# Optimization experiments

Measured on AMD Instinct MI355X. Metric: run time of the kernel, lower is better.

Reference implementation:

```python
import jax, jax.numpy as jnp
import numpy as np

EPS = 2e-5
N_ROT = 4  # p4 group: rotations by multiples of 90 degrees (exact via rot90)


def _conv2d(x, w, pad):
    # x: [B, Cin, H, W], w: [Cout, Cin, k, k]
    return jax.lax.conv_general_dilated(
        x, w, window_strides=(1, 1), padding=[(pad, pad), (pad, pad)],
        dimension_numbers=('NCHW', 'OIHW', 'NCHW'))


def _conv_rng(x, w):
    # Lifting (Rn -> G) conv. x: [B, I, H, W], w: [O, I, k, k] -> [B, O, 4, H', W']
    O, I, k, _ = w.shape
    wr = jnp.stack([jnp.rot90(w, r, axes=(-2, -1)) for r in range(N_ROT)])  # [4,O,I,k,k]
    y = _conv2d(x, wr.reshape(N_ROT * O, I, k, k), 0)  # [B, 4*O, H', W']
    B, _, H2, W2 = y.shape
    return y.reshape(B, N_ROT, O, H2, W2).transpose(0, 2, 1, 3, 4)


def _conv_gg(x, w, pad=0):
    # Group (G -> G) conv. x: [B, I, 4, H, W], w: [O, I, 4, k, k] -> [B, O, 4, H', W']
    O, I, _, k, _ = w.shape
    ws = []
    for r in range(N_ROT):
        wr = jnp.rot90(w, r, axes=(-2, -1))      # spatial rotation of the kernel
        wr = jnp.roll(wr, r, axis=2)              # cyclic shift of orientation axis
        ws.append(wr.reshape(O, I * N_ROT, k, k))
    wall = jnp.concatenate(ws, 0)                 # [4*O, I*4, k, k]
    B = x.shape[0]
    y = _conv2d(x.reshape(B, I * N_ROT, x.shape[-2], x.shape[-1]), wall, pad)
    H2, W2 = y.shape[-2:]
    return y.reshape(B, N_ROT, O, H2, W2).transpose(0, 2, 1, 3, 4)


def _att_rng(x, aw):
    # fSpatialAttention on Rn input: channel avg+max pooling -> 7x7 conv -> sigmoid gate.
    # x: [B, C, H, W], aw: [1, 2, 7, 7]
    pooled = jnp.concatenate([x.mean(1, keepdims=True), x.max(1, keepdims=True)], axis=1)
    att = jax.nn.sigmoid(_conv2d(pooled, aw, 3))  # [B,1,H,W], SAME padding
    return x * att


def _att_gg(x, aw):
    # fSpatialAttentionGG on G input: channel avg+max pooling -> equivariant 7x7 GG conv -> sigmoid.
    # x: [B, C, 4, H, W], aw: [1, 2, 4, 7, 7]
    pooled = jnp.concatenate([x.mean(1, keepdims=True), x.max(1, keepdims=True)], axis=1)
    att = jax.nn.sigmoid(_conv_gg(pooled, aw, pad=3))  # [B,1,4,H,W]
    return x * att


def _bn(x, g, b):
    # BatchNorm3d over [B, C, 4, H, W]: per-channel stats over (B, 4, H, W)
    m = x.mean((0, 2, 3, 4), keepdims=True)
    v = x.var((0, 2, 3, 4), keepdims=True)
    return (x - m) * jax.lax.rsqrt(v + EPS) * g.reshape(1, -1, 1, 1, 1) + b.reshape(1, -1, 1, 1, 1)


def _pool(x):
    # max_pooling_Rn: 2x2/2 spatial max pool applied independently per orientation
    return jax.lax.reduce_window(x, -jnp.inf, jax.lax.max,
                                 (1, 1, 1, 2, 2), (1, 1, 1, 2, 2), 'VALID')


def setup_inputs() -> dict:
    key = jax.random.key(0)
    ks = jax.random.split(key, 40)
    B, C = 2048, 10
    d = {'x': jax.random.normal(ks[0], (B, 1, 28, 28), jnp.float32)}
    d['c1_w'] = 0.2 * jax.random.normal(ks[1], (C, 1, 3, 3), jnp.float32)
    d['a1_w'] = 0.1 * jax.random.normal(ks[2], (1, 2, 7, 7), jnp.float32)
    j = 3
    for i in range(2, 7):
        d['c%d_w' % i] = 0.1 * jax.random.normal(ks[j], (C, C, 4, 3, 3), jnp.float32); j += 1
        d['a%d_w' % i] = 0.1 * jax.random.normal(ks[j], (1, 2, 4, 7, 7), jnp.float32); j += 1
    d['c7_w'] = 0.1 * jax.random.normal(ks[j], (10, C, 4, 4, 4), jnp.float32); j += 1
    d['a7_w'] = 0.1 * jax.random.normal(ks[j], (1, 2, 4, 7, 7), jnp.float32); j += 1
    for i in range(1, 7):
        d['bn%d_g' % i] = jnp.ones((C,), jnp.float32)
        d['bn%d_b' % i] = jnp.zeros((C,), jnp.float32)
    return d


def reference(x, c1_w, a1_w, c2_w, a2_w, c3_w, a3_w, c4_w, a4_w, c5_w, a5_w,
              c6_w, a6_w, c7_w, a7_w, bn1_g, bn1_b, bn2_g, bn2_b, bn3_g, bn3_b,
              bn4_g, bn4_b, bn5_g, bn5_b, bn6_g, bn6_b):
    # Dropout is treated as identity (eval mode / deterministic reference).
    out = jax.nn.relu(_bn(_conv_rng(_att_rng(x, a1_w), c1_w), bn1_g, bn1_b))      # [B,10,4,26,26]
    out = jax.nn.relu(_bn(_conv_gg(_att_gg(out, a2_w), c2_w), bn2_g, bn2_b))       # [B,10,4,24,24]
    out = _pool(out)                                                                # [B,10,4,12,12]
    out = jax.nn.relu(_bn(_conv_gg(_att_gg(out, a3_w), c3_w), bn3_g, bn3_b))       # 10x10
    out = jax.nn.relu(_bn(_conv_gg(_att_gg(out, a4_w), c4_w), bn4_g, bn4_b))       # 8x8
    out = jax.nn.relu(_bn(_conv_gg(_att_gg(out, a5_w), c5_w), bn5_g, bn5_b))       # 6x6
    out = jax.nn.relu(_bn(_conv_gg(_att_gg(out, a6_w), c6_w), bn6_g, bn6_b))       # 4x4
    out = _conv_gg(_att_gg(out, a7_w), c7_w)                                        # [B,10,4,1,1]
    out = out.max(axis=2)                                                           # group max-pool over orientations
    return out.reshape(out.shape[0], 10)
```

## Files before the change

kernel.cpp:

```cpp
#include <hip/hip_runtime.h>
#include <hip/hip_bf16.h>
#include <cstddef>

typedef __hip_bfloat16 bf;
typedef __attribute__((ext_vector_type(8))) short short8x;
typedef __attribute__((ext_vector_type(4))) float f32x4;

__device__ __forceinline__ float ldv(const float* p){ return *p; }
__device__ __forceinline__ float ldv(const bf* p){ return __bfloat162float(*p); }
__device__ __forceinline__ void stv(float* p, float v){ *p = v; }
__device__ __forceinline__ void stv(bf* p, float v){ *p = __float2bfloat16(v); }
__device__ __forceinline__ float sigm(float x){ return 1.f/(1.f + __expf(-x)); }
__device__ __forceinline__ short bfbits(float v){
  __hip_bfloat16 h = __float2bfloat16(v);
  return *(short*)&h;
}

__device__ __forceinline__ float ldin(const void* p, long i, int f32){
  return f32 ? ((const float*)p)[i] : __bfloat162float(((const bf*)p)[i]);
}

template<int K>
__device__ __forceinline__ int rot_src(int r, int t){
  int u = t / K, v = t % K;
  int s1 = v*K + (K-1-u);
  int s2 = (K-1-u)*K + (K-1-v);
  int s3 = (K-1-v)*K + u;
  return r==0 ? t : (r==1 ? s1 : (r==2 ? s2 : s3));
}

__global__ void k_detect(const void* x, int* ctrl){
  int lane = threadIdx.x;
  float mx = 0.f;
  for (int i = lane; i < 2048; i += 64){
    float v = __bfloat162float(((const bf*)x)[i]);
    if (v != v) v = 1e30f;
    mx = fmaxf(mx, fabsf(v));
  }
  #pragma unroll
  for (int off = 32; off > 0; off >>= 1) mx = fmaxf(mx, __shfl_xor(mx, off));
  if (lane == 0) ctrl[0] = (mx > 1e6f) ? 1 : 0;
}

__global__ __launch_bounds__(256) void k_build_bt(const void* c2, const void* c3, const void* c4,
                                                  const int* __restrict__ ctrl, short* __restrict__ btg){
  const void* ws[3] = {c2, c3, c4};
  const void* cw = ws[blockIdx.x];
  short* outp = btg + blockIdx.x * 17280;
  int f32 = ctrl[0];
  for (int i = threadIdx.x; i < 17280; i += 256){
    int t, n, k;
    if (i < 13824){
      t = i / 1536;
      int rem = i % 1536;
      int kq = rem / 384;
      n = (rem >> 3) % 48;
      k = kq*8 + (i & 7);
    } else {
      int j = i - 13824;
      t = j / 384;
      n = (j >> 3) % 48;
      k = 32 + (j & 7);
    }
    float v = 0.f;
    if (n < 40 && k < 40){
      int o = n >> 2, r = n & 3, ci = k >> 2, s = k & 3;
      v = ldin(cw, ((o*10 + ci)*4 + ((s - r) & 3))*9 + rot_src<3>(r, t), f32);
    }
    outp[i] = bfbits(v);
  }
}

__global__ __launch_bounds__(256) void k_l1(const void* __restrict__ x,
                                            const void* __restrict__ a1,
                                            const void* __restrict__ c1,
                                            const int* __restrict__ ctrl,
                                            float* __restrict__ xa,
                                            float* __restrict__ ssum, float* __restrict__ ssq){
  __shared__ float xs[784];
  __shared__ float ws[49];
  __shared__ float xg[28*29];
  __shared__ float wr1[360];
  __shared__ float lsum[16], lss[16];
  int b = blockIdx.x, tid = threadIdx.x;
  int f32 = ctrl[0];
  for (int i = tid; i < 784; i += 256) xs[i] = ldin(x, (long)b*784 + i, f32);
  if (tid < 49) ws[tid] = ldin(a1, tid, f32) + ldin(a1, 49 + tid, f32);
  for (int i = tid; i < 360; i += 256){
    int r = i / 90, rem = i % 90, o = rem / 9, t = rem % 9;
    wr1[i] = ldin(c1, o*9 + rot_src<3>(r, t), f32);
  }
  if (tid < 16){ lsum[tid] = 0.f; lss[tid] = 0.f; }
  __syncthreads();
  for (int p = tid; p < 784; p += 256){
    int h = p / 28, w = p % 28;
    float acc = 0.f;
    #pragma unroll
    for (int u = 0; u < 7; ++u){
      int hh = h + u - 3;
      if (hh < 0 || hh >= 28) continue;
      #pragma unroll
      for (int v = 0; v < 7; ++v){
        int ww = w + v - 3;
        if (ww < 0 || ww >= 28) continue;
        acc = fmaf(xs[hh*28 + ww], ws[u*7 + v], acc);
      }
    }
    float g = xs[p] * sigm(acc);
    xg[h*29 + w] = g;
    xa[(size_t)b*784 + p] = g;
  }
  __syncthreads();
  for (int it = tid; it < 1040; it += 256){
    int o = it / 104, rem = it % 104, r = rem / 26, h = rem % 26;
    float wt[9];
    #pragma unroll
    for (int t = 0; t < 9; ++t) wt[t] = wr1[(r*10 + o)*9 + t];
    float acc[26];
    #pragma unroll
    for (int w = 0; w < 26; ++w) acc[w] = 0.f;
    #pragma unroll
    for (int u = 0; u < 3; ++u){
      float rr[28];
      #pragma unroll
      for (int j = 0; j < 28; ++j) rr[j] = xg[(h + u)*29 + j];
      #pragma unroll
      for (int v = 0; v < 3; ++v){
        float wv = wt[u*3 + v];
        #pragma unroll
        for (int w = 0; w < 26; ++w) acc[w] = fmaf(rr[w + v], wv, acc[w]);
      }
    }
    float s1 = 0.f, s2 = 0.f;
    #pragma unroll
    for (int w = 0; w < 26; ++w){ s1 += acc[w]; s2 += acc[w]*acc[w]; }
    atomicAdd(&lsum[o], s1); atomicAdd(&lss[o], s2);
  }
  __syncthreads();
  if (tid < 10){ atomicAdd(&ssum[tid], lsum[tid]); atomicAdd(&ssq[tid], lss[tid]); }
}

__global__ void k_finalize(const float* __restrict__ ssum, const float* __restrict__ ssq,
                           const void* __restrict__ g, const void* __restrict__ bb,
                           const int* __restrict__ ctrl,
                           float invN, float* __restrict__ scale, float* __restrict__ shift){
  int c = threadIdx.x;
  if (c < 10){
    float m = ssum[c] * invN;
    float v = fmaxf(ssq[c] * invN - m*m, 0.f);
    float sc = ldin(g, c, ctrl[0]) * rsqrtf(v + 2e-5f);
    scale[c] = sc;
    shift[c] = ldin(bb, c, ctrl[0]) - m * sc;
  }
}

__global__ __launch_bounds__(128) void k_att2(const float* __restrict__ xa,
                                              const void* __restrict__ c1,
                                              const float* __restrict__ sc1,
                                              const float* __restrict__ sh1,
                                              const void* __restrict__ aw,
                                              const int* __restrict__ ctrl,
                                              float* __restrict__ attf){
  __shared__ float xs[28*29];
  __shared__ float wr1[360];
  __shared__ float ps[8*26*33];
  __shared__ float wl[1568];
  __shared__ float scs[10], shs[10];
  int b = blockIdx.x, tid = threadIdx.x;
  int f32 = ctrl[0];
  for (int i = tid; i < 784; i += 128){
    int row = i / 28, col = i % 28;
    xs[row*29 + col] = xa[(size_t)b*784 + i];
  }
  for (int i = tid; i < 360; i += 128){
    int r = i / 90, rem = i % 90, o = rem / 9, t = rem % 9;
    wr1[i] = ldin(c1, o*9 + rot_src<3>(r, t), f32);
  }
  for (int i = tid; i < 8*26*33; i += 128) ps[i] = 0.f;
  for (int i = tid; i < 1568; i += 128){
    int r = i / 392, rem = i % 392, i2 = rem / 196, s = (rem % 196)/49, t = rem % 49;
    int sp = (s - r) & 3;
    wl[i] = ldin(aw, (i2*4 + sp)*49 + rot_src<7>(r, t), f32);
  }
  if (tid < 10){ scs[tid] = sc1[tid]; shs[tid] = sh1[tid]; }
  __syncthreads();
  if (tid < 104){
    int s = tid / 26, h = tid % 26;
    float msum[26], mmax[26];
    #pragma unroll
    for (int w = 0; w < 26; ++w){ msum[w] = 0.f; mmax[w] = 0.f; }
    for (int o = 0; o < 10; ++o){
      const float* wb = wr1 + (s*10 + o)*9;
      float acc[26];
      #pragma unroll
      for (int w = 0; w < 26; ++w) acc[w] = 0.f;
      #pragma unroll
      for (int u = 0; u < 3; ++u){
        float rr[28];
        #pragma unroll
        for (int j = 0; j < 28; ++j) rr[j] = xs[(h + u)*29 + j];
        #pragma unroll
        for (int v = 0; v < 3; ++v){
          float wv = wb[u*3 + v];
          #pragma unroll
          for (int w = 0; w < 26; ++w) acc[w] = fmaf(rr[w + v], wv, acc[w]);
        }
      }
      float a_sc = scs[o], a_sh = shs[o];
      #pragma unroll
      for (int w = 0; w < 26; ++w){
        float val = fmaxf(fmaf(acc[w], a_sc, a_sh), 0.f);
        msum[w] += val; mmax[w] = fmaxf(mmax[w], val);
      }
    }
    #pragma unroll
    for (int w = 0; w < 26; ++w){
      ps[s*858 + h*33 + 3 + w] = msum[w] * 0.1f;
      ps[(4 + s)*858 + h*33 + 3 + w] = mmax[w];
    }
  }
  __syncthreads();
  if (tid < 104){
    int r = tid / 26, h = tid % 26;
    float acc[26];
    #pragma unroll
    for (int w = 0; w < 26; ++w) acc[w] = 0.f;
    for (int c = 0; c < 8; ++c){
      const float* wb = wl + r*392 + c*49;
      const float* pb = ps + c*858;
      #pragma unroll
      for (int u = 0; u < 7; ++u){
        int row = h + u - 3;
        if (row < 0 || row >= 26) continue;
        float rr[32];
        #pragma unroll
        for (int j = 0; j < 32; ++j) rr[j] = pb[row*33 + j];
        #pragma unroll
        for (int v = 0; v < 7; ++v){
          float wv = wb[u*7 + v];
          #pragma unroll
          for (int w = 0; w < 26; ++w) acc[w] = fmaf(rr[w + v], wv, acc[w]);
        }
      }
    }
    size_t base = ((size_t)b*4 + r)*676 + (size_t)h*26;
    #pragma unroll
    for (int w = 0; w < 26; ++w) attf[base + w] = sigm(acc[w]);
  }
}

__global__ __launch_bounds__(512, 4) void k_conv2m(const float* __restrict__ xa,
                                                const void* __restrict__ c1,
                                                const float* __restrict__ sc1,
                                                const float* __restrict__ sh1,
                                                const float* __restrict__ attm,
                                                const short* __restrict__ btg,
                                                const int* __restrict__ ctrl,
                                                bf* __restrict__ ap2,
                                                float* __restrict__ ssum, float* __restrict__ ssq){
  __shared__ alignas(16) float xs2[784];
  __shared__ float wr1[360];
  __shared__ alignas(16) float attL[4*676];
  __shared__ alignas(16) short xin[676*40];
  __shared__ float lsum[16], lss[16];
  int tid = threadIdx.x, b = blockIdx.x;
  int f32 = ctrl[0];
  for (int i = tid; i < 784; i += 512) xs2[i] = xa[(size_t)b*784 + i];
  for (int i = tid; i < 360; i += 512){
    int r = i / 90, rem = i % 90, o = rem / 9, t = rem % 9;
    wr1[i] = ldin(c1, o*9 + rot_src<3>(r, t), f32);
  }
  for (int i = tid; i < 2704; i += 512) attL[i] = attm[(size_t)b*2704 + i];
  if (tid < 16){ lsum[tid] = 0.f; lss[tid] = 0.f; }
  __syncthreads();
  for (int it = tid; it < 1040; it += 512){
    int row = it / 40, ch = it % 40;
    int ci = ch >> 2, s = ch & 3;
    float wt[9];
    {
      const float* wb = wr1 + (s*10 + ci)*9;
      #pragma unroll
      for (int t = 0; t < 9; ++t) wt[t] = wb[t];
    }
    float sc = sc1[ci], sh = sh1[ci];
    float acc[26];
    #pragma unroll
    for (int w = 0; w < 26; ++w) acc[w] = 0.f;
    #pragma unroll
    for (int u = 0; u < 3; ++u){
      float rr[28];
      const float4* rp = (const float4*)(xs2 + (row + u)*28);
      #pragma unroll
      for (int j = 0; j < 7; ++j){ float4 q = rp[j]; rr[4*j]=q.x; rr[4*j+1]=q.y; rr[4*j+2]=q.z; rr[4*j+3]=q.w; }
      #pragma unroll
      for (int v = 0; v < 3; ++v){
        float wv = wt[u*3 + v];
        #pragma unroll
        for (int w = 0; w < 26; ++w) acc[w] = fmaf(rr[w + v], wv, acc[w]);
      }
    }
    const float* ap = attL + s*676 + row*26;
    #pragma unroll
    for (int w = 0; w < 26; ++w){
      float v = fmaxf(fmaf(acc[w], sc, sh), 0.f) * ap[w];
      xin[(row*26 + w)*40 + ch] = bfbits(v);
    }
  }
  __syncthreads();

  int wv = tid >> 6, lane = tid & 63, lm = lane & 15, lq = lane >> 4;
  short8x z8 = {0,0,0,0,0,0,0,0};
  short8x b32[9], bt1[9];
  int curNt = -1, n = 0, o = 0;
  for (int u = wv; u < 54; u += 8){
    int nt = u / 18, mp = u % 18;
    if (nt != curNt){
      curNt = nt; n = nt*16 + lm; o = n >> 2;
      #pragma unroll
      for (int t = 0; t < 9; ++t){
        b32[t] = *(const short8x*)(btg + (((t*4 + lq)*48 + n) << 3));
        bt1[t] = z8;
        if (lq == 0) bt1[t] = *(const short8x*)(btg + 13824 + ((t*48 + n) << 3));
      }
    }
    int mt0 = mp*2, mt1 = mp*2 + 1;
    int mA0 = mt0*16 + lm, mA1 = mt1*16 + lm;
    int qi0 = mA0 >> 2, sub0 = mA0 & 3;
    int h00 = 2*(qi0/12) + (sub0 >> 1), w00 = 2*(qi0%12) + (sub0 & 1);
    int qi1 = mA1 >> 2, sub1 = mA1 & 3;
    int h01 = 2*(qi1/12) + (sub1 >> 1), w01 = 2*(qi1%12) + (sub1 & 1);
    f32x4 acc0 = {0.f,0.f,0.f,0.f}, acc1 = {0.f,0.f,0.f,0.f};
    #pragma unroll
    for (int t = 0; t < 9; ++t){
      int sp0 = (h00 + t/3)*26 + (w00 + t%3);
      int sp1 = (h01 + t/3)*26 + (w01 + t%3);
      short8x a00 = *(const short8x*)&xin[sp0*40 + lq*8];
      short8x a01 = *(const short8x*)&xin[sp1*40 + lq*8];
      short8x a10 = z8, a11 = z8;
      if (lq == 0){
        a10 = *(const short8x*)&xin[sp0*40 + 32];
        a11 = *(const short8x*)&xin[sp1*40 + 32];
      }
      acc0 = __builtin_amdgcn_mfma_f32_16x16x32_bf16(a00, b32[t], acc0, 0, 0, 0);
      acc1 = __builtin_amdgcn_mfma_f32_16x16x32_bf16(a01, b32[t], acc1, 0, 0, 0);
      acc0 = __builtin_amdgcn_mfma_f32_16x16x32_bf16(a10, bt1[t], acc0, 0, 0, 0);
      acc1 = __builtin_amdgcn_mfma_f32_16x16x32_bf16(a11, bt1[t], acc1, 0, 0, 0);
    }
    if (n < 40){
      float s1 = acc0[0]+acc0[1]+acc0[2]+acc0[3] + acc1[0]+acc1[1]+acc1[2]+acc1[3];
      float s2 = acc0[0]*acc0[0]+acc0[1]*acc0[1]+acc0[2]*acc0[2]+acc0[3]*acc0[3]
               + acc1[0]*acc1[0]+acc1[1]*acc1[1]+acc1[2]*acc1[2]+acc1[3]*acc1[3];
      atomicAdd(&lsum[o], s1); atomicAdd(&lss[o], s2);
      float mx0 = fmaxf(fmaxf(acc0[0], acc0[1]), fmaxf(acc0[2], acc0[3]));
      float mx1 = fmaxf(fmaxf(acc1[0], acc1[1]), fmaxf(acc1[2], acc1[3]));
      size_t pbase = ((size_t)b*40 + n)*144;
      stv(ap2 + pbase + mt0*4 + lq, mx0);
      stv(ap2 + pbase + mt1*4 + lq, mx1);
    }
  }
  __syncthreads();
  if (tid < 10){ atomicAdd(&ssum[tid], lsum[tid]); atomicAdd(&ssq[tid], lss[tid]); }
}

template<int HIN, int WIN, int NT, typename TI>
__global__ __launch_bounds__(NT) void k_conv_ggm(const TI* __restrict__ act,
                                                 const float* __restrict__ scale,
                                                 const float* __restrict__ shift,
                                                 const float* __restrict__ attm,
                                                 const short* __restrict__ btg,
                                                 float* __restrict__ out,
                                                 float* __restrict__ ssum, float* __restrict__ ssq){
  constexpr int HOUT = HIN - 2, WOUT = WIN - 2;
  constexpr int M = HOUT*WOUT, HW = HIN*WIN;
  constexpr int MT = (M + 15)/16, MU = (MT + 1)/2, UNITS = MU*3;
  constexpr int NWV = NT/64;
  __shared__ alignas(16) short xin[HW*40];
  __shared__ float lsum[16], lss[16];
  int tid = threadIdx.x, b = blockIdx.x;
  if (tid < 16){ lsum[tid] = 0.f; lss[tid] = 0.f; }
  for (int i = tid; i < HW*40; i += NT){
    int sp = i / 40, ch = i % 40;
    int ci = ch >> 2, s = ch & 3;
    float a = ldv(act + ((size_t)b*40 + ch)*HW + sp);
    a = fmaxf(fmaf(a, scale[ci], shift[ci]), 0.f);
    xin[i] = bfbits(a * attm[((size_t)b*4 + s)*HW + sp]);
  }
  __syncthreads();
  int wv = tid >> 6, lane = tid & 63, lm = lane & 15, lq = lane >> 4;
  short8x z8 = {0,0,0,0,0,0,0,0};
  short8x b32[9], bt1[9];
  int curNt = -1, n = 0, o = 0;
  for (int u = wv; u < UNITS; u += NWV){
    int nt = u / MU, mu = u % MU;
    if (nt != curNt){
      curNt = nt; n = nt*16 + lm; o = n >> 2;
      #pragma unroll
      for (int t = 0; t < 9; ++t){
        b32[t] = *(const short8x*)(btg + (((t*4 + lq)*48 + n) << 3));
        bt1[t] = z8;
        if (lq == 0) bt1[t] = *(const short8x*)(btg + 13824 + ((t*48 + n) << 3));
      }
    }
    int mt0 = mu*2, mt1 = mu*2 + 1;
    int mA0 = mt0*16 + lm; if (mA0 > M-1) mA0 = M-1;
    int mA1 = mt1*16 + lm; if (mA1 > M-1) mA1 = M-1;
    int mh0 = mA0 / WOUT, mw0 = mA0 % WOUT;
    int mh1 = mA1 / WOUT, mw1 = mA1 % WOUT;
    f32x4 acc0 = {0.f,0.f,0.f,0.f}, acc1 = {0.f,0.f,0.f,0.f};
    #pragma unroll
    for (int t = 0; t < 9; ++t){
      int sp0 = (mh0 + t/3)*WIN + (mw0 + t%3);
      int sp1 = (mh1 + t/3)*WIN + (mw1 + t%3);
      short8x a00 = *(const short8x*)&xin[sp0*40 + lq*8];
      short8x a01 = *(const short8x*)&xin[sp1*40 + lq*8];
      short8x a10 = z8, a11 = z8;
      if (lq == 0){
        a10 = *(const short8x*)&xin[sp0*40 + 32];
        a11 = *(const short8x*)&xin[sp1*40 + 32];
      }
      acc0 = __builtin_amdgcn_mfma_f32_16x16x32_bf16(a00, b32[t], acc0, 0, 0, 0);
      acc1 = __builtin_amdgcn_mfma_f32_16x16x32_bf16(a01, b32[t], acc1, 0, 0, 0);
      acc0 = __builtin_amdgcn_mfma_f32_16x16x32_bf16(a10, bt1[t], acc0, 0, 0, 0);
      acc1 = __builtin_amdgcn_mfma_f32_16x16x32_bf16(a11, bt1[t], acc1, 0, 0, 0);
    }
    if (n < 40){
      float s1 = 0.f, s2 = 0.f;
      size_t obase = ((size_t)b*40 + n)*M;
      #pragma unroll
      for (int reg = 0; reg < 4; ++reg){
        int m0 = mt0*16 + lq*4 + reg;
        if (m0 < M){ float v = acc0[reg]; s1 += v; s2 += v*v; out[obase + m0] = v; }
        int m1 = mt1*16 + lq*4 + reg;
        if (m1 < M){ float v = acc1[reg]; s1 += v; s2 += v*v; out[obase + m1] = v; }
      }
      atomicAdd(&lsum[o], s1); atomicAdd(&lss[o], s2);
    }
  }
  __syncthreads();
  if (tid < 10){ atomicAdd(&ssum[tid], lsum[tid]); atomicAdd(&ssq[tid], lss[tid]); }
}

template<int H, int W, int NT, typename TA>
__global__ __launch_bounds__(NT) void k_att_gg(const TA* __restrict__ act,
                                               const float* __restrict__ scale,
                                               const float* __restrict__ shift,
                                               const void* __restrict__ aw,
                                               const int* __restrict__ ctrl,
                                               float* __restrict__ att){
  constexpr int WG = (W + 6) | 1;
  constexpr int HW = H*W;
  __shared__ float ps[8*H*WG];
  __shared__ float wl[1568];
  int b = blockIdx.x, tid = threadIdx.x;
  int f32 = ctrl[0];
  for (int i = tid; i < 4*H*WG; i += NT){
    int s = i / (H*WG), rem = i % (H*WG), row = rem / WG, col = rem % WG;
    int cc = col - 3;
    float mn = 0.f, mx = 0.f;
    if (cc >= 0 && cc < W){
      float sum = 0.f; mx = 0.f;
      const TA* ap = act + (size_t)b*40*HW + (size_t)s*HW + row*W + cc;
      #pragma unroll
      for (int c = 0; c < 10; ++c){
        float v = fmaxf(fmaf(ldv(ap + (size_t)c*4*HW), scale[c], shift[c]), 0.f);
        sum += v; mx = fmaxf(mx, v);
      }
      mn = sum * 0.1f;
    }
    ps[s*H*WG + row*WG + col] = mn;
    ps[(4 + s)*H*WG + row*WG + col] = mx;
  }
  for (int i = tid; i < 1568; i += NT){
    int r = i / 392, rem = i % 392, i2 = rem / 196, s = (rem % 196)/49, t = rem % 49;
    int sp = (s - r) & 3;
    wl[i] = ldin(aw, (i2*4 + sp)*49 + rot_src<7>(r, t), f32);
  }
  __syncthreads();
  for (int it = tid; it < 4*H; it += NT){
    int r = it / H, h = it % H;
    float acc[W];
    #pragma unroll
    for (int w = 0; w < W; ++w) acc[w] = 0.f;
    for (int c = 0; c < 8; ++c){
      const float* wb = wl + r*392 + c*49;
      const float* pb = ps + c*H*WG;
      #pragma unroll
      for (int u = 0; u < 7; ++u){
        int row = h + u - 3;
        if (row < 0 || row >= H) continue;
        float rr[W + 6];
        #pragma unroll
        for (int j = 0; j < W + 6; ++j) rr[j] = pb[row*WG + j];
        #pragma unroll
        for (int v = 0; v < 7; ++v){
          float wv = wb[u*7 + v];
          #pragma unroll
          for (int w = 0; w < W; ++w) acc[w] = fmaf(rr[w + v], wv, acc[w]);
        }
      }
    }
    size_t base = ((size_t)b*4 + r)*HW + (size_t)h*W;
    #pragma unroll
    for (int w = 0; w < W; ++w) att[base + w] = sigm(acc[w]);
  }
}

template<int HIN, int WIN, int K, int SR, int NT, bool STATS, typename TI, typename TO>
__global__ __launch_bounds__(NT) void k_conv_gg(const TI* __restrict__ act,
                                                const float* __restrict__ scale,
                                                const float* __restrict__ shift,
                                                const float* __restrict__ attm,
                                                const void* __restrict__ cw,
                                                const int* __restrict__ ctrl,
                                                TO* __restrict__ out,
                                                float* __restrict__ ssum, float* __restrict__ ssq){
  constexpr int HOUT = HIN - K + 1;
  constexpr int WOUT = WIN - K + 1;
  constexpr int NS   = HOUT / SR;
  constexpr int WP   = WIN | 1;
  constexpr int NW   = 10*10*4*K*K;
  __shared__ float xin[40*HIN*WP];
  __shared__ float wl[NW];
  __shared__ float lsum[16], lss[16];
  int tid = threadIdx.x;
  int b = blockIdx.x;
  int f32 = ctrl[0];
  for (int i = tid; i < 40*HIN*WP; i += NT){
    int c = i / (HIN*WP), rem = i % (HIN*WP), rr = rem / WP, col = rem % WP;
    float v = 0.f;
    if (col < WIN){
      int ch = c >> 2, s = c & 3;
      float a = ldv(act + ((size_t)b*40 + c)*HIN*WIN + (size_t)rr*WIN + col);
      a = fmaxf(fmaf(a, scale[ch], shift[ch]), 0.f);
      v = a * attm[((size_t)b*4 + s)*HIN*WIN + (size_t)rr*WIN + col];
    }
    xin[i] = v;
  }
  for (int i = tid; i < NW; i += NT) wl[i] = ldin(cw, i, f32);
  if (STATS && tid < 16){ lsum[tid] = 0.f; lss[tid] = 0.f; }
  __syncthreads();
  for (int it = tid; it < 40*NS; it += NT){
    int o = it / (4*NS), rem = it % (4*NS), r = rem / NS, hs = rem % NS;
    int h0 = hs * SR;
    int perm[K*K];
    #pragma unroll
    for (int t = 0; t < K*K; ++t) perm[t] = rot_src<K>(r, t);
    float acc[SR][WOUT];
    #pragma unroll
    for (int a = 0; a < SR; ++a)
      #pragma unroll
      for (int w = 0; w < WOUT; ++w) acc[a][w] = 0.f;
    for (int ci = 0; ci < 10; ++ci){
      #pragma unroll
      for (int s = 0; s < 4; ++s){
        int sp = (s - r) & 3;
        const float* wb = wl + (size_t)((o*10 + ci)*4 + sp)*K*K;
        float wt[K*K];
        #pragma unroll
        for (int t = 0; t < K*K; ++t) wt[t] = wb[perm[t]];
        const float* ib = xin + (ci*4 + s)*HIN*WP;
        #pragma unroll
        for (int ri = 0; ri < SR + K - 1; ++ri){
          float rr[WP];
          #pragma unroll
          for (int j = 0; j < WP; ++j) rr[j] = ib[(h0 + ri)*WP + j];
          #pragma unroll
          for (int u = 0; u < K; ++u){
            int orr = ri - u;
            if (orr < 0 || orr >= SR) continue;
            #pragma unroll
            for (int v = 0; v < K; ++v){
              float wv = wt[u*K + v];
              #pragma unroll
              for (int w = 0; w < WOUT; ++w) acc[orr][w] = fmaf(rr[w + v], wv, acc[orr][w]);
            }
          }
        }
      }
    }
    if (STATS){
      float s1 = 0.f, s2 = 0.f;
      #pragma unroll
      for (int a = 0; a < SR; ++a)
        #pragma unroll
        for (int w = 0; w < WOUT; ++w){ s1 += acc[a][w]; s2 += acc[a][w]*acc[a][w]; }
      atomicAdd(&lsum[o], s1); atomicAdd(&lss[o], s2);
    }
    #pragma unroll
    for (int a = 0; a < SR; ++a){
      size_t base = ((size_t)b*40 + o*4 + r)*HOUT*WOUT + (size_t)(h0 + a)*WOUT;
      #pragma unroll
      for (int w = 0; w < WOUT; ++w) stv(out + base + w, acc[a][w]);
    }
  }
  if (STATS){
    __syncthreads();
    if (tid < 10){ atomicAdd(&ssum[tid], lsum[tid]); atomicAdd(&ssq[tid], lss[tid]); }
  }
}

__global__ __launch_bounds__(256) void k_out_max(const float* __restrict__ y7, void* __restrict__ outp,
                                                 const int* __restrict__ ctrl){
  int idx = blockIdx.x * 256 + threadIdx.x;
  if (idx >= 20480) return;
  int f32 = ctrl[0];
  const float* p = y7 + (size_t)idx*4;
  float m = fmaxf(fmaxf(p[0], p[1]), fmaxf(p[2], p[3]));
  if (f32) ((float*)outp)[idx] = m;
  else stv((bf*)outp + idx, m);
}

extern "C" void kernel_launch(void* const* d_in, const int* in_sizes, int n_in,
                              void* d_out, int out_size, void* d_ws, size_t ws_size,
                              hipStream_t stream){
  (void)in_sizes; (void)n_in; (void)out_size; (void)ws_size;
  const void* x  = d_in[0];
  const void* c1 = d_in[1];
  const void* a1 = d_in[2];
  const void* c2 = d_in[3];
  const void* a2 = d_in[4];
  const void* c3 = d_in[5];
  const void* a3 = d_in[6];
  const void* c4 = d_in[7];
  const void* a4 = d_in[8];
  const void* c5 = d_in[9];
  const void* a5 = d_in[10];
  const void* c6 = d_in[11];
  const void* a6 = d_in[12];
  const void* c7 = d_in[13];
  const void* a7 = d_in[14];
  const void* bng[6] = {d_in[15],d_in[17],d_in[19],d_in[21],d_in[23],d_in[25]};
  const void* bnb[6] = {d_in[16],d_in[18],d_in[20],d_in[22],d_in[24],d_in[26]};

  size_t off = 0;
  char* wsb = (char*)d_ws;
  auto alloc = [&](size_t bytes)->void*{ void* p = wsb + off; off += (bytes + 255) & ~(size_t)255; return p; };
  int*   ctrl   = (int*)alloc(256);
  float* stats  = (float*)alloc(192*sizeof(float));
  float* scales = (float*)alloc(192*sizeof(float));
  short* btfr   = (short*)alloc(3*17280*2);
  char*  region1 = (char*)alloc(28573696);
  bf*    ap2 = (bf*)alloc((size_t)2048*40*144*2);
  float* yD  = (float*)alloc((size_t)2048*40*100*4);
  float* xa    = (float*)region1;
  float* attf2 = (float*)(region1 + 6422528);
  float* yE    = (float*)region1;
  float* attf3 = (float*)(region1 + 20971520);

  hipMemsetAsync(ctrl, 0, 1024, stream);
  k_detect<<<1, 64, 0, stream>>>(x, ctrl);
  k_build_bt<<<3, 256, 0, stream>>>(c2, c3, c4, ctrl, btfr);

  k_l1<<<2048, 256, 0, stream>>>(x, a1, c1, ctrl, xa, stats + 0, stats + 16);
  k_finalize<<<1, 64, 0, stream>>>(stats + 0, stats + 16, bng[0], bnb[0], ctrl, 1.f/5537792.f, scales + 0, scales + 16);

  k_att2<<<2048, 128, 0, stream>>>(xa, c1, scales + 0, scales + 16, a2, ctrl, attf2);
  k_conv2m<<<2048, 512, 0, stream>>>(xa, c1, scales + 0, scales + 16, attf2, btfr, ctrl, ap2, stats + 32, stats + 48);
  k_finalize<<<1, 64, 0, stream>>>(stats + 32, stats + 48, bng[1], bnb[1], ctrl, 1.f/4718592.f, scales + 32, scales + 48);

  k_att_gg<12,12,64,bf><<<2048, 64, 0, stream>>>(ap2, scales + 32, scales + 48, a3, ctrl, attf3);
  k_conv_ggm<12,12,256,bf><<<2048, 256, 0, stream>>>(ap2, scales + 32, scales + 48,
                                                     attf3, btfr + 17280, yD, stats + 64, stats + 80);
  k_finalize<<<1, 64, 0, stream>>>(stats + 64, stats + 80, bng[2], bnb[2], ctrl, 1.f/819200.f, scales + 64, scales + 80);

  k_att_gg<10,10,64,float><<<2048, 64, 0, stream>>>(yD, scales + 64, scales + 80, a4, ctrl, attf3);
  k_conv_ggm<10,10,128,float><<<2048, 128, 0, stream>>>(yD, scales + 64, scales + 80,
                                                        attf3, btfr + 34560, yE, stats + 96, stats + 112);
  k_finalize<<<1, 64, 0, stream>>>(stats + 96, stats + 112, bng[3], bnb[3], ctrl, 1.f/524288.f, scales + 96, scales + 112);

  k_att_gg<8,8,64,float><<<2048, 64, 0, stream>>>(yE, scales + 96, scales + 112, a5, ctrl, attf3);
  k_conv_gg<8,8,3,2,192,true,float,float><<<2048, 192, 0, stream>>>(yE, scales + 96, scales + 112,
                                                                attf3, c5, ctrl, yD, stats + 128, stats + 144);
  k_finalize<<<1, 64, 0, stream>>>(stats + 128, stats + 144, bng[4], bnb[4], ctrl, 1.f/294912.f, scales + 128, scales + 144);

  k_att_gg<6,6,64,float><<<2048, 64, 0, stream>>>(yD, scales + 128, scales + 144, a6, ctrl, attf3);
  k_conv_gg<6,6,3,2,128,true,float,float><<<2048, 128, 0, stream>>>(yD, scales + 128, scales + 144,
                                                                attf3, c6, ctrl, yE, stats + 160, stats + 176);
  k_finalize<<<1, 64, 0, stream>>>(stats + 160, stats + 176, bng[5], bnb[5], ctrl, 1.f/131072.f, scales + 160, scales + 176);

  k_att_gg<4,4,64,float><<<2048, 64, 0, stream>>>(yE, scales + 160, scales + 176, a7, ctrl, attf3);
  k_conv_gg<4,4,4,1,64,false,float,float><<<2048, 64, 0, stream>>>(yE, scales + 160, scales + 176,
                                                                attf3, c7, ctrl, yD, (float*)nullptr, (float*)nullptr);
  k_out_max<<<80, 256, 0, stream>>>(yD, d_out, ctrl);
}
```

Measured before the change: 983.8 us.

## Fuse group spatial attention into the following GG conv kernels for layers 3-6

```diff
diff --git a/kernel.cpp b/kernel.cpp
--- a/kernel.cpp
+++ b/kernel.cpp
@@ -362,28 +362,85 @@
   if (tid < 10){ atomicAdd(&ssum[tid], lsum[tid]); atomicAdd(&ssq[tid], lss[tid]); }
 }
 
-template<int HIN, int WIN, int NT, typename TI>
-__global__ __launch_bounds__(NT) void k_conv_ggm(const TI* __restrict__ act,
-                                                 const float* __restrict__ scale,
-                                                 const float* __restrict__ shift,
-                                                 const float* __restrict__ attm,
-                                                 const short* __restrict__ btg,
-                                                 float* __restrict__ out,
-                                                 float* __restrict__ ssum, float* __restrict__ ssq){
-  constexpr int HOUT = HIN - 2, WOUT = WIN - 2;
-  constexpr int M = HOUT*WOUT, HW = HIN*WIN;
+template<int HIN, int NT, typename TI>
+__global__ __launch_bounds__(NT) void k_fusedm(const TI* __restrict__ act,
+                                               const float* __restrict__ scale,
+                                               const float* __restrict__ shift,
+                                               const void* __restrict__ aw,
+                                               const short* __restrict__ btg,
+                                               const int* __restrict__ ctrl,
+                                               float* __restrict__ out,
+                                               float* __restrict__ ssum, float* __restrict__ ssq){
+  constexpr int HOUT = HIN - 2, WOUT = HIN - 2;
+  constexpr int M = HOUT*WOUT, HW = HIN*HIN;
+  constexpr int WG = (HIN + 6) | 1;
   constexpr int MT = (M + 15)/16, MU = (MT + 1)/2, UNITS = MU*3;
   constexpr int NWV = NT/64;
+  __shared__ float xf[HW*41];
+  __shared__ float ps[8*HIN*WG];
+  __shared__ float wl[1568];
+  __shared__ float attL[4*HW];
   __shared__ alignas(16) short xin[HW*40];
   __shared__ float lsum[16], lss[16];
   int tid = threadIdx.x, b = blockIdx.x;
+  int f32 = ctrl[0];
   if (tid < 16){ lsum[tid] = 0.f; lss[tid] = 0.f; }
+  for (int i = tid; i < 8*HIN*WG; i += NT) ps[i] = 0.f;
+  for (int i = tid; i < 1568; i += NT){
+    int r = i / 392, rem = i % 392, i2 = rem / 196, s = (rem % 196)/49, t = rem % 49;
+    int sp = (s - r) & 3;
+    wl[i] = ldin(aw, (i2*4 + sp)*49 + rot_src<7>(r, t), f32);
+  }
+  for (int i = tid; i < 40*HW; i += NT){
+    int ch = i / HW, sp = i % HW;
+    int ci = ch >> 2;
+    float a = ldv(act + ((size_t)b*40 + ch)*HW + sp);
+    xf[sp*41 + ch] = fmaxf(fmaf(a, scale[ci], shift[ci]), 0.f);
+  }
+  __syncthreads();
+  for (int i = tid; i < 4*HW; i += NT){
+    int s = i / HW, sp = i % HW;
+    float sum = 0.f, mx = 0.f;
+    #pragma unroll
+    for (int ci = 0; ci < 10; ++ci){
+      float v = xf[sp*41 + ci*4 + s];
+      sum += v; mx = fmaxf(mx, v);
+    }
+    int row = sp / HIN, col = sp % HIN;
+    ps[s*HIN*WG + row*WG + 3 + col] = sum * 0.1f;
+    ps[(4 + s)*HIN*WG + row*WG + 3 + col] = mx;
+  }
+  __syncthreads();
+  for (int it = tid; it < 4*HIN; it += NT){
+    int r = it / HIN, h = it % HIN;
+    float acc[HIN];
+    #pragma unroll
+    for (int w = 0; w < HIN; ++w) acc[w] = 0.f;
+    for (int c = 0; c < 8; ++c){
+      const float* wb = wl + r*392 + c*49;
+      const float* pb = ps + c*HIN*WG;
+      #pragma unroll
+      for (int u = 0; u < 7; ++u){
+        int row = h + u - 3;
+        if (row < 0 || row >= HIN) continue;
+        float rr[HIN + 6];
+        #pragma unroll
+        for (int j = 0; j < HIN + 6; ++j) rr[j] = pb[row*WG + j];
+        #pragma unroll
+        for (int v = 0; v < 7; ++v){
+          float wv = wb[u*7 + v];
+          #pragma unroll
+          for (int w = 0; w < HIN; ++w) acc[w] = fmaf(rr[w + v], wv, acc[w]);
+        }
+      }
+    }
+    #pragma unroll
+    for (int w = 0; w < HIN; ++w) attL[r*HW + h*HIN + w] = sigm(acc[w]);
+  }
+  __syncthreads();
   for (int i = tid; i < HW*40; i += NT){
     int sp = i / 40, ch = i % 40;
-    int ci = ch >> 2, s = ch & 3;
-    float a = ldv(act + ((size_t)b*40 + ch)*HW + sp);
-    a = fmaxf(fmaf(a, scale[ci], shift[ci]), 0.f);
-    xin[i] = bfbits(a * attm[((size_t)b*4 + s)*HW + sp]);
+    xin[i] = bfbits(xf[sp*41 + ch] * attL[(ch & 3)*HW + sp]);
   }
   __syncthreads();
   int wv = tid >> 6, lane = tid & 63, lm = lane & 15, lq = lane >> 4;
@@ -409,8 +466,8 @@
     f32x4 acc0 = {0.f,0.f,0.f,0.f}, acc1 = {0.f,0.f,0.f,0.f};
     #pragma unroll
     for (int t = 0; t < 9; ++t){
-      int sp0 = (mh0 + t/3)*WIN + (mw0 + t%3);
-      int sp1 = (mh1 + t/3)*WIN + (mw1 + t%3);
+      int sp0 = (mh0 + t/3)*HIN + (mw0 + t%3);
+      int sp1 = (mh1 + t/3)*HIN + (mw1 + t%3);
       short8x a00 = *(const short8x*)&xin[sp0*40 + lq*8];
       short8x a01 = *(const short8x*)&xin[sp1*40 + lq*8];
       short8x a10 = z8, a11 = z8;
@@ -434,6 +491,152 @@
         if (m1 < M){ float v = acc1[reg]; s1 += v; s2 += v*v; out[obase + m1] = v; }
       }
       atomicAdd(&lsum[o], s1); atomicAdd(&lss[o], s2);
+    }
+  }
+  __syncthreads();
+  if (tid < 10){ atomicAdd(&ssum[tid], lsum[tid]); atomicAdd(&ssq[tid], lss[tid]); }
+}
+
+template<int HIN, int SR, int NT>
+__global__ __launch_bounds__(NT) void k_fusedf(const float* __restrict__ act,
+                                               const float* __restrict__ scale,
+                                               const float* __restrict__ shift,
+                                               const void* __restrict__ aw,
+                                               const void* __restrict__ cw,
+                                               const int* __restrict__ ctrl,
+                                               float* __restrict__ out,
+                                               float* __restrict__ ssum, float* __restrict__ ssq){
+  constexpr int K = 3;
+  constexpr int WIN = HIN;
+  constexpr int HOUT = HIN - 2, WOUT = HIN - 2;
+  constexpr int NS = HOUT / SR;
+  constexpr int WP = WIN | 1;
+  constexpr int XP = HIN*WP + 1;
+  constexpr int HW = HIN*WIN;
+  constexpr int WG = (WIN + 6) | 1;
+  __shared__ float xf[40*XP];
+  __shared__ float wl[3600];
+  __shared__ float wla[1568];
+  __shared__ float ps[8*HIN*WG];
+  __shared__ float attL[4*HW];
+  __shared__ float lsum[16], lss[16];
+  int tid = threadIdx.x, b = blockIdx.x;
+  int f32 = ctrl[0];
+  if (tid < 16){ lsum[tid] = 0.f; lss[tid] = 0.f; }
+  for (int i = tid; i < 8*HIN*WG; i += NT) ps[i] = 0.f;
+  for (int i = tid; i < 3600; i += NT) wl[i] = ldin(cw, i, f32);
+  for (int i = tid; i < 1568; i += NT){
+    int r = i / 392, rem = i % 392, i2 = rem / 196, s = (rem % 196)/49, t = rem % 49;
+    int sp = (s - r) & 3;
+    wla[i] = ldin(aw, (i2*4 + sp)*49 + rot_src<7>(r, t), f32);
+  }
+  for (int i = tid; i < 40*HIN*WP; i += NT){
+    int c = i / (HIN*WP), rem = i % (HIN*WP), rr = rem / WP, col = rem % WP;
+    float v = 0.f;
+    if (col < WIN){
+      int ch = c >> 2;
+      float a = ldv(act + ((size_t)b*40 + c)*HW + (size_t)rr*WIN + col);
+      v = fmaxf(fmaf(a, scale[ch], shift[ch]), 0.f);
+    }
+    xf[c*XP + rr*WP + col] = v;
+  }
+  __syncthreads();
+  for (int i = tid; i < 4*HW; i += NT){
+    int s = i / HW, sp = i % HW;
+    int row = sp / WIN, col = sp % WIN;
+    float sum = 0.f, mx = 0.f;
+    #pragma unroll
+    for (int ci = 0; ci < 10; ++ci){
+      float v = xf[(ci*4 + s)*XP + row*WP + col];
+      sum += v; mx = fmaxf(mx, v);
+    }
+    ps[s*HIN*WG + row*WG + 3 + col] = sum * 0.1f;
+    ps[(4 + s)*HIN*WG + row*WG + 3 + col] = mx;
+  }
+  __syncthreads();
+  for (int it = tid; it < 4*HIN; it += NT){
+    int r = it / HIN, h = it % HIN;
+    float acc[WIN];
+    #pragma unroll
+    for (int w = 0; w < WIN; ++w) acc[w] = 0.f;
+    for (int c = 0; c < 8; ++c){
+      const float* wb = wla + r*392 + c*49;
+      const float* pb = ps + c*HIN*WG;
+      #pragma unroll
+      for (int u = 0; u < 7; ++u){
+        int row = h + u - 3;
+        if (row < 0 || row >= HIN) continue;
+        float rr[WIN + 6];
+        #pragma unroll
+        for (int j = 0; j < WIN + 6; ++j) rr[j] = pb[row*WG + j];
+        #pragma unroll
+        for (int v = 0; v < 7; ++v){
+          float wv = wb[u*7 + v];
+          #pragma unroll
+          for (int w = 0; w < WIN; ++w) acc[w] = fmaf(rr[w + v], wv, acc[w]);
+        }
+      }
+    }
+    #pragma unroll
+    for (int w = 0; w < WIN; ++w) attL[r*HW + h*WIN + w] = sigm(acc[w]);
+  }
+  __syncthreads();
+  for (int i = tid; i < 40*HW; i += NT){
+    int c = i / HW, sp = i % HW;
+    int row = sp / WIN, col = sp % WIN;
+    xf[c*XP + row*WP + col] *= attL[(c & 3)*HW + sp];
+  }
+  __syncthreads();
+  for (int it = tid; it < 40*NS; it += NT){
+    int o = it / (4*NS), rem = it % (4*NS), r = rem / NS, hs = rem % NS;
+    int h0 = hs * SR;
+    int perm[9];
+    #pragma unroll
+    for (int t = 0; t < 9; ++t) perm[t] = rot_src<3>(r, t);
+    float acc[SR][WOUT];
+    #pragma unroll
+    for (int a = 0; a < SR; ++a)
+      #pragma unroll
+      for (int w = 0; w < WOUT; ++w) acc[a][w] = 0.f;
+    for (int ci = 0; ci < 10; ++ci){
+      #pragma unroll
+      for (int s = 0; s < 4; ++s){
+        int sp = (s - r) & 3;
+        const float* wb = wl + (size_t)((o*10 + ci)*4 + sp)*9;
+        float wt[9];
+        #pragma unroll
+        for (int t = 0; t < 9; ++t) wt[t] = wb[perm[t]];
+        const float* ib = xf + (ci*4 + s)*XP;
+        #pragma unroll
+        for (int ri = 0; ri < SR + K - 1; ++ri){
+          float rr[WP];
+          #pragma unroll
+          for (int j = 0; j < WP; ++j) rr[j] = ib[(h0 + ri)*WP + j];
+          #pragma unroll
+          for (int u = 0; u < K; ++u){
+            int orr = ri - u;
+            if (orr < 0 || orr >= SR) continue;
+            #pragma unroll
+            for (int v = 0; v < K; ++v){
+              float wv = wt[u*K + v];
+              #pragma unroll
+              for (int w = 0; w < WOUT; ++w) acc[orr][w] = fmaf(rr[w + v], wv, acc[orr][w]);
+            }
+          }
+        }
+      }
+    }
+    float s1 = 0.f, s2 = 0.f;
+    #pragma unroll
+    for (int a = 0; a < SR; ++a)
+      #pragma unroll
+      for (int w = 0; w < WOUT; ++w){ s1 += acc[a][w]; s2 += acc[a][w]*acc[a][w]; }
+    atomicAdd(&lsum[o], s1); atomicAdd(&lss[o], s2);
+    #pragma unroll
+    for (int a = 0; a < SR; ++a){
+      size_t base = ((size_t)b*40 + o*4 + r)*HOUT*WOUT + (size_t)(h0 + a)*WOUT;
+      #pragma unroll
+      for (int w = 0; w < WOUT; ++w) out[base + w] = acc[a][w];
     }
   }
   __syncthreads();
@@ -658,24 +861,20 @@
   k_conv2m<<<2048, 512, 0, stream>>>(xa, c1, scales + 0, scales + 16, attf2, btfr, ctrl, ap2, stats + 32, stats + 48);
   k_finalize<<<1, 64, 0, stream>>>(stats + 32, stats + 48, bng[1], bnb[1], ctrl, 1.f/4718592.f, scales + 32, scales + 48);
 
-  k_att_gg<12,12,64,bf><<<2048, 64, 0, stream>>>(ap2, scales + 32, scales + 48, a3, ctrl, attf3);
-  k_conv_ggm<12,12,256,bf><<<2048, 256, 0, stream>>>(ap2, scales + 32, scales + 48,
-                                                     attf3, btfr + 17280, yD, stats + 64, stats + 80);
+  k_fusedm<12,256,bf><<<2048, 256, 0, stream>>>(ap2, scales + 32, scales + 48, a3, btfr + 17280, ctrl,
+                                                yD, stats + 64, stats + 80);
   k_finalize<<<1, 64, 0, stream>>>(stats + 64, stats + 80, bng[2], bnb[2], ctrl, 1.f/819200.f, scales + 64, scales + 80);
 
-  k_att_gg<10,10,64,float><<<2048, 64, 0, stream>>>(yD, scales + 64, scales + 80, a4, ctrl, attf3);
-  k_conv_ggm<10,10,128,float><<<2048, 128, 0, stream>>>(yD, scales + 64, scales + 80,
-                                                        attf3, btfr + 34560, yE, stats + 96, stats + 112);
+  k_fusedm<10,256,float><<<2048, 256, 0, stream>>>(yD, scales + 64, scales + 80, a4, btfr + 34560, ctrl,
+                                                   yE, stats + 96, stats + 112);
   k_finalize<<<1, 64, 0, stream>>>(stats + 96, stats + 112, bng[3], bnb[3], ctrl, 1.f/524288.f, scales + 96, scales + 112);
 
-  k_att_gg<8,8,64,float><<<2048, 64, 0, stream>>>(yE, scales + 96, scales + 112, a5, ctrl, attf3);
-  k_conv_gg<8,8,3,2,192,true,float,float><<<2048, 192, 0, stream>>>(yE, scales + 96, scales + 112,
-                                                                attf3, c5, ctrl, yD, stats + 128, stats + 144);
+  k_fusedf<8,2,192><<<2048, 192, 0, stream>>>(yE, scales + 96, scales + 112, a5, c5, ctrl,
+                                              yD, stats + 128, stats + 144);
   k_finalize<<<1, 64, 0, stream>>>(stats + 128, stats + 144, bng[4], bnb[4], ctrl, 1.f/294912.f, scales + 128, scales + 144);
 
-  k_att_gg<6,6,64,float><<<2048, 64, 0, stream>>>(yD, scales + 128, scales + 144, a6, ctrl, attf3);
-  k_conv_gg<6,6,3,2,128,true,float,float><<<2048, 128, 0, stream>>>(yD, scales + 128, scales + 144,
-                                                                attf3, c6, ctrl, yE, stats + 160, stats + 176);
+  k_fusedf<6,2,128><<<2048, 128, 0, stream>>>(yD, scales + 128, scales + 144, a6, c6, ctrl,
+                                              yE, stats + 160, stats + 176);
   k_finalize<<<1, 64, 0, stream>>>(stats + 160, stats + 176, bng[5], bnb[5], ctrl, 1.f/131072.f, scales + 160, scales + 176);
 
   k_att_gg<4,4,64,float><<<2048, 64, 0, stream>>>(yE, scales + 160, scales + 176, a7, ctrl, attf3);
```

New measurement: 1.011 ms. +2.8%, slower.
